# Performance work log

Measured on AMD Instinct MI355X. Metric: run time of the kernel, lower is better.

Reference implementation:

```python
import jax, jax.numpy as jnp
import numpy as np

NUM_CODES = 8192
DIM = 512
COMMITMENT_COST = 0.25


def setup_inputs() -> dict:
    key = jax.random.key(0)
    kx, kc = jax.random.split(key)
    x = jax.random.normal(kx, (8, 4096, DIM), dtype=jnp.float32)
    # nn.init.uniform_(codebook.weight, -1/num_codes, 1/num_codes)
    bound = 1.0 / NUM_CODES
    codebook = jax.random.uniform(kc, (NUM_CODES, DIM), dtype=jnp.float32,
                                  minval=-bound, maxval=bound)
    return {"x": x, "codebook": codebook}


def reference(x, codebook):
    orig_shape = x.shape
    flat = x.reshape(-1, orig_shape[-1])              # [N, D]
    # Squared-distance expansion (argmin-equivalent to torch.cdist's L2):
    # ||f||^2 - 2 f.c + ||c||^2
    x_sq = jnp.sum(flat * flat, axis=-1, keepdims=True)          # [N, 1]
    c_sq = jnp.sum(codebook * codebook, axis=-1)                 # [K]
    dists = x_sq - 2.0 * jnp.einsum('nd,kd->nk', flat, codebook) + c_sq  # [N, K]
    indices_flat = jnp.argmin(dists, axis=-1)                    # [N] int
    quantized_flat = codebook[indices_flat]                      # [N, D]
    # codebook_loss = mse(quantized, sg(flat)); commitment = mse(flat, sg(quantized))
    codebook_loss = jnp.mean((quantized_flat - jax.lax.stop_gradient(flat)) ** 2)
    commitment_loss = jnp.mean((flat - jax.lax.stop_gradient(quantized_flat)) ** 2)
    vq_loss = codebook_loss + COMMITMENT_COST * commitment_loss
    # straight-through
    quantized_st = flat + jax.lax.stop_gradient(quantized_flat - flat)
    return (quantized_st.reshape(orig_shape), vq_loss,
            indices_flat.reshape(orig_shape[:-1]))
```

## Files before the change

kernel.cpp:

```cpp
#include <hip/hip_runtime.h>


#define NROWS 32768
#define KCODES 8192
#define DD 512
#define CAP 24
#define MARGIN 2.5e-4f

typedef __bf16 bf16_t;
typedef __bf16 bf16x8 __attribute__((ext_vector_type(8)));
typedef float f32x4 __attribute__((ext_vector_type(4)));

__device__ __forceinline__ int lofs(int row, int s) {
  return row * 32 + (((s ^ ((row >> 1) & 3))) << 3);
}

__device__ __forceinline__ void gld16(const bf16_t* g, bf16_t* l) {
  __builtin_amdgcn_global_load_lds(
      (const __attribute__((address_space(1))) void*)g,
      (__attribute__((address_space(3))) void*)l, 16, 0, 0);
}

__global__ __launch_bounds__(256) void prep_kernel(const float* __restrict__ in,
                                                   float* __restrict__ out_sq,
                                                   bf16_t* __restrict__ outb,
                                                   int nrows) {
  const int wave = threadIdx.x >> 6;
  const int lane = threadIdx.x & 63;
  const int row = blockIdx.x * 4 + wave;
  if (row >= nrows) return;
  const float* p = in + (size_t)row * DD;
  double s = 0.0;
#pragma unroll
  for (int j = 0; j < DD / 64; ++j) {
    float v = p[j * 64 + lane];
    float sq = v * v;
    s += (double)sq;
  }
  for (int off = 32; off > 0; off >>= 1) s += __shfl_down(s, off, 64);
  if (lane == 0) out_sq[row] = (float)s;
  const float4* p4 = (const float4*)p;
  float4 a = p4[lane * 2];
  float4 b = p4[lane * 2 + 1];
  bf16x8 o = {(bf16_t)a.x, (bf16_t)a.y, (bf16_t)a.z, (bf16_t)a.w,
              (bf16_t)b.x, (bf16_t)b.y, (bf16_t)b.z, (bf16_t)b.w};
  *(bf16x8*)(outb + (size_t)row * DD + lane * 8) = o;
}

__global__ __launch_bounds__(256, 2) void coarse_kernel(
    const bf16_t* __restrict__ xbf, const bf16_t* __restrict__ cbbf,
    const float* __restrict__ csq, unsigned char* __restrict__ cnt_g,
    unsigned short* __restrict__ list_g, unsigned* __restrict__ bmin_g) {
  __shared__ bf16_t As[4][128 * 32];
  __shared__ bf16_t Bs[4][128 * 32];
  __shared__ unsigned best[128];
  __shared__ int cnt_l[128];
  __shared__ unsigned short list_l[128 * CAP];

  const int tid = threadIdx.x;
  const int w = tid >> 6;
  const int lane = tid & 63;
  const int q = lane >> 4;
  const int l15 = lane & 15;
  const int rOff = (w & 1) * 64;
  const int cOff = (w >> 1) * 64;

  const int bid = blockIdx.x;
  const int xcd = bid & 7;
  const int g = bid >> 3;
  const int qtr = xcd >> 1;
  const int rowblk = (xcd & 1) * 128 + g;
  const int row0 = rowblk * 128;
  const int cbase = qtr * (KCODES / 4);
  const int NCI = (KCODES / 4) / 128;

  for (int i = tid; i < 128; i += 256) { best[i] = 0xFFFFFFFFu; cnt_l[i] = 0; }

  const int sub = lane >> 2;
  const int pos = lane & 3;
  const bf16_t *agp[2], *bgp[2];
  int aofs[2], bofs[2];
#pragma unroll
  for (int a = 0; a < 2; ++a) {
    const int row = w * 32 + a * 16 + sub;
    const int sg = pos ^ ((row >> 1) & 3);
    agp[a] = xbf + (size_t)(row0 + row) * DD + sg * 8;
    aofs[a] = row * 32 + pos * 8;
    bgp[a] = cbbf + (size_t)(cbase + row) * DD + sg * 8;
    bofs[a] = row * 32 + pos * 8;
  }

  int afofs[4], bfofs[4];
#pragma unroll
  for (int rt = 0; rt < 4; ++rt) afofs[rt] = lofs(rOff + rt * 16 + l15, q);
#pragma unroll
  for (int ct = 0; ct < 4; ++ct) bfofs[ct] = lofs(cOff + ct * 16 + l15, q);

  auto issue_step = [&](int sN, int buf) {
    const int kbN = (sN & (DD / 32 - 1)) * 32;
    const size_t coffN = (size_t)((sN >> 4) & (NCI - 1)) * (128 * DD);
    gld16(agp[0] + kbN, &As[buf][aofs[0]]);
    gld16(agp[1] + kbN, &As[buf][aofs[1]]);
    gld16(bgp[0] + coffN + kbN, &Bs[buf][bofs[0]]);
    gld16(bgp[1] + coffN + kbN, &Bs[buf][bofs[1]]);
  };

  issue_step(0, 0);
  issue_step(1, 1);
  issue_step(2, 2);
  asm volatile("s_waitcnt vmcnt(8) lgkmcnt(0)" ::: "memory");
  __builtin_amdgcn_sched_barrier(0);
  __builtin_amdgcn_s_barrier();
  __builtin_amdgcn_sched_barrier(0);

  f32x4 acc[4][4];

#define PIPE_STEP(S, J)                                                       \
  do {                                                                        \
    issue_step((S) + 3, ((J) + 3) & 3);                                       \
    bf16x8 af[4], bfr[4];                                                     \
    _Pragma("unroll") for (int rt = 0; rt < 4; ++rt)                          \
        af[rt] = *(const bf16x8*)&As[(J)][afofs[rt]];                         \
    _Pragma("unroll") for (int ct = 0; ct < 4; ++ct)                          \
        bfr[ct] = *(const bf16x8*)&Bs[(J)][bfofs[ct]];                        \
    _Pragma("unroll") for (int rt = 0; rt < 4; ++rt)                          \
        _Pragma("unroll") for (int ct = 0; ct < 4; ++ct)                      \
            acc[rt][ct] = __builtin_amdgcn_mfma_f32_16x16x32_bf16(            \
                af[rt], bfr[ct], acc[rt][ct], 0, 0, 0);                       \
    asm volatile("s_waitcnt vmcnt(8)" ::: "memory");                          \
    __builtin_amdgcn_sched_barrier(0);                                        \
    __builtin_amdgcn_s_barrier();                                             \
    __builtin_amdgcn_sched_barrier(0);                                        \
  } while (0)

#pragma unroll 1
  for (int ci = 0; ci < NCI; ++ci) {
    const int c0 = cbase + ci * 128;
#pragma unroll
    for (int rt = 0; rt < 4; ++rt)
#pragma unroll
      for (int ct = 0; ct < 4; ++ct) {
        f32x4 z = {0.f, 0.f, 0.f, 0.f};
        acc[rt][ct] = z;
      }

#pragma unroll 1
    for (int kc4 = 0; kc4 < 4; ++kc4) {
      const int s = ci * 16 + kc4 * 4;
      PIPE_STEP(s + 0, 0);
      PIPE_STEP(s + 1, 1);
      PIPE_STEP(s + 2, 2);
      PIPE_STEP(s + 3, 3);
    }

    float cs1[4];
#pragma unroll
    for (int ct = 0; ct < 4; ++ct)
      cs1[ct] = 1.0f + csq[c0 + cOff + ct * 16 + l15];

#pragma unroll
    for (int rt = 0; rt < 4; ++rt) {
#pragma unroll
      for (int reg = 0; reg < 4; ++reg) {
        float m = fmaf(-2.0f, acc[rt][0][reg], cs1[0]);
#pragma unroll
        for (int ct = 1; ct < 4; ++ct) {
          float d = fmaf(-2.0f, acc[rt][ct][reg], cs1[ct]);
          m = fminf(m, d);
        }
        unsigned mb = __float_as_uint(m);
#pragma unroll
        for (int msk = 1; msk <= 8; msk <<= 1) {
          unsigned o = __shfl_xor(mb, msk, 64);
          mb = mb < o ? mb : o;
        }
        if (l15 == 0) atomicMin(&best[rOff + rt * 16 + q * 4 + reg], mb);
      }
    }
    asm volatile("s_waitcnt lgkmcnt(0)" ::: "memory");
    __builtin_amdgcn_sched_barrier(0);
    __builtin_amdgcn_s_barrier();
    __builtin_amdgcn_sched_barrier(0);

#pragma unroll
    for (int rt = 0; rt < 4; ++rt) {
#pragma unroll
      for (int reg = 0; reg < 4; ++reg) {
        const int rloc = rOff + rt * 16 + q * 4 + reg;
        const float thr = __uint_as_float(best[rloc]) + MARGIN;
#pragma unroll
        for (int ct = 0; ct < 4; ++ct) {
          float d = fmaf(-2.0f, acc[rt][ct][reg], cs1[ct]);
          if (d <= thr) {
            int pos2 = atomicAdd(&cnt_l[rloc], 1);
            if (pos2 < CAP)
              list_l[rloc * CAP + pos2] =
                  (unsigned short)(c0 + cOff + ct * 16 + l15);
          }
        }
      }
    }
  }
#undef PIPE_STEP

  __syncthreads();

  for (int i = tid; i < 128; i += 256) {
    int c = cnt_l[i];
    cnt_g[(size_t)(row0 + i) * 4 + qtr] = (unsigned char)(c > CAP ? CAP + 1 : c);
    bmin_g[(size_t)(row0 + i) * 4 + qtr] = best[i];
  }
  for (int i = tid; i < 128 * CAP; i += 256) {
    const int r = i / CAP, p = i % CAP;
    list_g[((size_t)(row0 + r) * 4 + qtr) * CAP + p] = list_l[i];
  }
}

__device__ __forceinline__ float exact_dist(const float4* __restrict__ xr4,
                                            const float* __restrict__ cb,
                                            const float* __restrict__ csq,
                                            float xs, int idx) {
  const float4* cr4 = (const float4*)(cb + (size_t)idx * DD);
  float acc = 0.0f;
  for (int k4 = 0; k4 < DD / 4; ++k4) {
    float4 xv = xr4[k4];
    float4 cv = cr4[k4];
    acc = fmaf(xv.x, cv.x, acc);
    acc = fmaf(xv.y, cv.y, acc);
    acc = fmaf(xv.z, cv.z, acc);
    acc = fmaf(xv.w, cv.w, acc);
  }
  float t = xs - 2.0f * acc;
  return t + csq[idx];
}

__global__ __launch_bounds__(256) void rescore_epilogue_kernel(
    const float* __restrict__ x, const float* __restrict__ cb,
    const float* __restrict__ xsq, const float* __restrict__ csq,
    const unsigned short* __restrict__ list,
    const unsigned char* __restrict__ cnt, const unsigned* __restrict__ bmin,
    float* __restrict__ out_q, float* __restrict__ out_idx_f,
    double* __restrict__ partials) {
  const int row = blockIdx.x * 4 + (threadIdx.x >> 6);
  const int lane = threadIdx.x & 63;
  const unsigned char* c4 = cnt + (size_t)row * 4;
  const unsigned* bm4 = bmin + (size_t)row * 4;
  const float xs = xsq[row];
  const float4* xr4 = (const float4*)(x + (size_t)row * DD);

  float qm[4];
  int n[4];
#pragma unroll
  for (int s = 0; s < 4; ++s) {
    qm[s] = __uint_as_float(bm4[s]);
    n[s] = c4[s];
  }
  const float gmin = fminf(fminf(qm[0], qm[1]), fminf(qm[2], qm[3]));
  const float cut = gmin + MARGIN;
  bool listed[4], scanq[4];
  int L = 0;
#pragma unroll
  for (int s = 0; s < 4; ++s) {
    const bool rel = (qm[s] <= cut);
    listed[s] = rel && (n[s] <= CAP);
    scanq[s] = rel && (n[s] > CAP);
    if (listed[s]) L += n[s];
  }
  if (L > 64) {
#pragma unroll
    for (int s = 0; s < 4; ++s)
      if (listed[s]) { listed[s] = false; scanq[s] = true; }
    L = 0;
  }

  unsigned long long bestv = ~0ULL;

  int myidx = -1;
  int base = 0;
#pragma unroll
  for (int s = 0; s < 4; ++s) {
    if (listed[s]) {
      if (myidx < 0 && lane >= base && lane < base + n[s])
        myidx = (int)list[((size_t)row * 4 + s) * CAP + (lane - base)];
      base += n[s];
    }
  }
  if (myidx >= 0) {
    float d = exact_dist(xr4, cb, csq, xs, myidx);
    bestv = ((unsigned long long)__float_as_uint(d) << 32) | (unsigned)myidx;
  }

#pragma unroll
  for (int s = 0; s < 4; ++s) {
    if (scanq[s]) {
      const int q0 = s * (KCODES / 4);
      for (int idx = q0 + lane; idx < q0 + KCODES / 4; idx += 64) {
        float d = exact_dist(xr4, cb, csq, xs, idx);
        unsigned long long pk =
            ((unsigned long long)__float_as_uint(d) << 32) | (unsigned)idx;
        if (pk < bestv) bestv = pk;
      }
    }
  }

#pragma unroll
  for (int s = 1; s <= 32; s <<= 1) {
    unsigned long long o = __shfl_xor(bestv, s, 64);
    if (o < bestv) bestv = o;
  }
  const int k = (int)(bestv & 0xffffffffu);

  const float4* qr = (const float4*)(cb + (size_t)k * DD);
  float4* orow = (float4*)(out_q + (size_t)row * DD);

  float4 xa = xr4[lane], qa = qr[lane];
  float dax = qa.x - xa.x, day = qa.y - xa.y, daz = qa.z - xa.z, daw = qa.w - xa.w;
  float4 oa;
  oa.x = xa.x + dax; oa.y = xa.y + day; oa.z = xa.z + daz; oa.w = xa.w + daw;
  orow[lane] = oa;
  double pa = (double)(dax * dax) + (double)(day * day) +
              (double)(daz * daz) + (double)(daw * daw);

  float4 xb = xr4[lane + 64], qb = qr[lane + 64];
  float dbx = qb.x - xb.x, dby = qb.y - xb.y, dbz = qb.z - xb.z, dbw = qb.w - xb.w;
  float4 ob;
  ob.x = xb.x + dbx; ob.y = xb.y + dby; ob.z = xb.z + dbz; ob.w = xb.w + dbw;
  orow[lane + 64] = ob;
  double pb = (double)(dbx * dbx) + (double)(dby * dby) +
              (double)(dbz * dbz) + (double)(dbw * dbw);

  for (int off = 32; off > 0; off >>= 1) pa += __shfl_down(pa, off, 64);
  for (int off = 32; off > 0; off >>= 1) pb += __shfl_down(pb, off, 64);
  if (lane == 0) {
    partials[row] = pa + pb;
    out_idx_f[row] = (float)k;
  }
}

__global__ __launch_bounds__(256) void finalize_kernel(
    const double* __restrict__ partials, float* __restrict__ out_loss) {
  __shared__ double red[256];
  double s = 0.0;
  for (int i = threadIdx.x; i < NROWS; i += 256) s += partials[i];
  red[threadIdx.x] = s;
  __syncthreads();
  for (int st = 128; st > 0; st >>= 1) {
    if (threadIdx.x < st) red[threadIdx.x] += red[threadIdx.x + st];
    __syncthreads();
  }
  if (threadIdx.x == 0) {
    double mean = red[0] / ((double)NROWS * (double)DD);
    float cl = (float)mean;
    out_loss[0] = cl + 0.25f * cl;
  }
}

extern "C" void kernel_launch(void* const* d_in, const int* in_sizes, int n_in,
                              void* d_out, int out_size, void* d_ws,
                              size_t ws_size, hipStream_t stream) {
  const float* x = (const float*)d_in[0];
  const float* cb = (const float*)d_in[1];
  float* out = (float*)d_out;

  char* ws = (char*)d_ws;
  double* partials = (double*)ws;
  float* csq = (float*)(ws + 262144);
  float* xsq = (float*)(ws + 262144 + 32768);
  unsigned char* cnt = (unsigned char*)(ws + 262144 + 32768 + 131072);
  unsigned* bmin = (unsigned*)(ws + 262144 + 32768 + 131072 + 131072);
  unsigned short* list =
      (unsigned short*)(ws + 262144 + 32768 + 131072 + 131072 + 524288);

  bf16_t* cbbf = (bf16_t*)d_out;
  bf16_t* xbf = cbbf + (size_t)KCODES * DD;

  prep_kernel<<<KCODES / 4, 256, 0, stream>>>(cb, csq, cbbf, KCODES);
  prep_kernel<<<NROWS / 4, 256, 0, stream>>>(x, xsq, xbf, NROWS);
  coarse_kernel<<<1024, 256, 0, stream>>>(xbf, cbbf, csq, cnt, list, bmin);
  rescore_epilogue_kernel<<<NROWS / 4, 256, 0, stream>>>(
      x, cb, xsq, csq, list, cnt, bmin, out, out + 16777216 + 1, partials);
  finalize_kernel<<<1, 256, 0, stream>>>(partials, out + 16777216);
}
```

Baseline: 1.007 ms.

## Replace 4-stage LDS pipeline with single-buffer 64-wide K tiles, raise occupancy

The coarse bf16 GEMM kernel drops its 4-deep ring of 32-wide K slices fed by async global_load_lds. It now uses one 128x64 shared tile per operand with a new XOR swizzle, loaded between two __syncthreads, and each tile feeds two MFMA passes. Shared memory per block roughly halves, so launch bounds go from 2 to 3 blocks per CU. The aim is to hide memory latency through more resident workgroups instead of explicit software pipelining. The risk is that load latency is now exposed inside each block on every K tile, and the tighter register budget could cause spills.

```diff
diff --git a/kernel.cpp b/kernel.cpp
--- a/kernel.cpp
+++ b/kernel.cpp
@@ -10,10 +10,6 @@
 typedef __bf16 bf16_t;
 typedef __bf16 bf16x8 __attribute__((ext_vector_type(8)));
 typedef float f32x4 __attribute__((ext_vector_type(4)));
-
-__device__ __forceinline__ int lofs(int row, int s) {
-  return row * 32 + (((s ^ ((row >> 1) & 3))) << 3);
-}
 
 __device__ __forceinline__ void gld16(const bf16_t* g, bf16_t* l) {
   __builtin_amdgcn_global_load_lds(
@@ -47,12 +43,12 @@
   *(bf16x8*)(outb + (size_t)row * DD + lane * 8) = o;
 }
 
-__global__ __launch_bounds__(256, 2) void coarse_kernel(
+__global__ __launch_bounds__(256, 3) void coarse_kernel(
     const bf16_t* __restrict__ xbf, const bf16_t* __restrict__ cbbf,
     const float* __restrict__ csq, unsigned char* __restrict__ cnt_g,
     unsigned short* __restrict__ list_g, unsigned* __restrict__ bmin_g) {
-  __shared__ bf16_t As[4][128 * 32];
-  __shared__ bf16_t Bs[4][128 * 32];
+  __shared__ bf16_t As[128 * 64];
+  __shared__ bf16_t Bs[128 * 64];
   __shared__ unsigned best[128];
   __shared__ int cnt_l[128];
   __shared__ unsigned short list_l[128 * CAP];
@@ -76,66 +72,40 @@
 
   for (int i = tid; i < 128; i += 256) { best[i] = 0xFFFFFFFFu; cnt_l[i] = 0; }
 
-  const int sub = lane >> 2;
-  const int pos = lane & 3;
-  const bf16_t *agp[2], *bgp[2];
-  int aofs[2], bofs[2];
-#pragma unroll
-  for (int a = 0; a < 2; ++a) {
-    const int row = w * 32 + a * 16 + sub;
-    const int sg = pos ^ ((row >> 1) & 3);
-    agp[a] = xbf + (size_t)(row0 + row) * DD + sg * 8;
-    aofs[a] = row * 32 + pos * 8;
-    bgp[a] = cbbf + (size_t)(cbase + row) * DD + sg * 8;
-    bofs[a] = row * 32 + pos * 8;
+  const int srow = tid >> 3;
+  const int spos = tid & 7;
+  const int sg = spos ^ (srow & 7);
+  const bf16_t *aG[4], *bG[4];
+  bf16_t *aL[4], *bL[4];
+#pragma unroll
+  for (int c = 0; c < 4; ++c) {
+    const int r = c * 32 + srow;
+    aG[c] = xbf + (size_t)(row0 + r) * DD + sg * 8;
+    bG[c] = cbbf + (size_t)(cbase + r) * DD + sg * 8;
+    aL[c] = As + r * 64 + spos * 8;
+    bL[c] = Bs + r * 64 + spos * 8;
   }
 
   int afofs[4], bfofs[4];
 #pragma unroll
-  for (int rt = 0; rt < 4; ++rt) afofs[rt] = lofs(rOff + rt * 16 + l15, q);
-#pragma unroll
-  for (int ct = 0; ct < 4; ++ct) bfofs[ct] = lofs(cOff + ct * 16 + l15, q);
-
-  auto issue_step = [&](int sN, int buf) {
-    const int kbN = (sN & (DD / 32 - 1)) * 32;
-    const size_t coffN = (size_t)((sN >> 4) & (NCI - 1)) * (128 * DD);
-    gld16(agp[0] + kbN, &As[buf][aofs[0]]);
-    gld16(agp[1] + kbN, &As[buf][aofs[1]]);
-    gld16(bgp[0] + coffN + kbN, &Bs[buf][bofs[0]]);
-    gld16(bgp[1] + coffN + kbN, &Bs[buf][bofs[1]]);
-  };
-
-  issue_step(0, 0);
-  issue_step(1, 1);
-  issue_step(2, 2);
-  asm volatile("s_waitcnt vmcnt(8) lgkmcnt(0)" ::: "memory");
-  __builtin_amdgcn_sched_barrier(0);
-  __builtin_amdgcn_s_barrier();
-  __builtin_amdgcn_sched_barrier(0);
+  for (int rt = 0; rt < 4; ++rt) {
+    const int r = rOff + rt * 16 + l15;
+    afofs[rt] = r * 64 + ((q ^ (r & 7)) << 3);
+  }
+#pragma unroll
+  for (int ct = 0; ct < 4; ++ct) {
+    const int r = cOff + ct * 16 + l15;
+    bfofs[ct] = r * 64 + ((q ^ (r & 7)) << 3);
+  }
+
+  __syncthreads();
 
   f32x4 acc[4][4];
-
-#define PIPE_STEP(S, J)                                                       \
-  do {                                                                        \
-    issue_step((S) + 3, ((J) + 3) & 3);                                       \
-    bf16x8 af[4], bfr[4];                                                     \
-    _Pragma("unroll") for (int rt = 0; rt < 4; ++rt)                          \
-        af[rt] = *(const bf16x8*)&As[(J)][afofs[rt]];                         \
-    _Pragma("unroll") for (int ct = 0; ct < 4; ++ct)                          \
-        bfr[ct] = *(const bf16x8*)&Bs[(J)][bfofs[ct]];                        \
-    _Pragma("unroll") for (int rt = 0; rt < 4; ++rt)                          \
-        _Pragma("unroll") for (int ct = 0; ct < 4; ++ct)                      \
-            acc[rt][ct] = __builtin_amdgcn_mfma_f32_16x16x32_bf16(            \
-                af[rt], bfr[ct], acc[rt][ct], 0, 0, 0);                       \
-    asm volatile("s_waitcnt vmcnt(8)" ::: "memory");                          \
-    __builtin_amdgcn_sched_barrier(0);                                        \
-    __builtin_amdgcn_s_barrier();                                             \
-    __builtin_amdgcn_sched_barrier(0);                                        \
-  } while (0)
 
 #pragma unroll 1
   for (int ci = 0; ci < NCI; ++ci) {
     const int c0 = cbase + ci * 128;
+    const size_t cioff = (size_t)(ci * 128) * DD;
 #pragma unroll
     for (int rt = 0; rt < 4; ++rt)
 #pragma unroll
@@ -145,12 +115,41 @@
       }
 
 #pragma unroll 1
-    for (int kc4 = 0; kc4 < 4; ++kc4) {
-      const int s = ci * 16 + kc4 * 4;
-      PIPE_STEP(s + 0, 0);
-      PIPE_STEP(s + 1, 1);
-      PIPE_STEP(s + 2, 2);
-      PIPE_STEP(s + 3, 3);
+    for (int kc = 0; kc < DD / 64; ++kc) {
+      const int kb = kc * 64;
+      __syncthreads();
+#pragma unroll
+      for (int c = 0; c < 4; ++c) {
+        gld16(aG[c] + kb, aL[c]);
+        gld16(bG[c] + cioff + kb, bL[c]);
+      }
+      __syncthreads();
+
+      bf16x8 a0[4], b0[4];
+#pragma unroll
+      for (int rt = 0; rt < 4; ++rt) a0[rt] = *(const bf16x8*)&As[afofs[rt]];
+#pragma unroll
+      for (int ct = 0; ct < 4; ++ct) b0[ct] = *(const bf16x8*)&Bs[bfofs[ct]];
+#pragma unroll
+      for (int rt = 0; rt < 4; ++rt)
+#pragma unroll
+        for (int ct = 0; ct < 4; ++ct)
+          acc[rt][ct] = __builtin_amdgcn_mfma_f32_16x16x32_bf16(
+              a0[rt], b0[ct], acc[rt][ct], 0, 0, 0);
+
+      bf16x8 a1[4], b1[4];
+#pragma unroll
+      for (int rt = 0; rt < 4; ++rt)
+        a1[rt] = *(const bf16x8*)&As[afofs[rt] ^ 32];
+#pragma unroll
+      for (int ct = 0; ct < 4; ++ct)
+        b1[ct] = *(const bf16x8*)&Bs[bfofs[ct] ^ 32];
+#pragma unroll
+      for (int rt = 0; rt < 4; ++rt)
+#pragma unroll
+        for (int ct = 0; ct < 4; ++ct)
+          acc[rt][ct] = __builtin_amdgcn_mfma_f32_16x16x32_bf16(
+              a1[rt], b1[ct], acc[rt][ct], 0, 0, 0);
     }
 
     float cs1[4];
@@ -177,10 +176,7 @@
         if (l15 == 0) atomicMin(&best[rOff + rt * 16 + q * 4 + reg], mb);
       }
     }
-    asm volatile("s_waitcnt lgkmcnt(0)" ::: "memory");
-    __builtin_amdgcn_sched_barrier(0);
-    __builtin_amdgcn_s_barrier();
-    __builtin_amdgcn_sched_barrier(0);
+    __syncthreads();
 
 #pragma unroll
     for (int rt = 0; rt < 4; ++rt) {
@@ -201,7 +197,6 @@
       }
     }
   }
-#undef PIPE_STEP
 
   __syncthreads();
 
```

Result: faster. 896.7 us (-10.9%).
